# Performance work log

Measured on AMD Instinct MI355X. Metric: run time of the kernel, lower is better.

## Reference

```python
import jax, jax.numpy as jnp
import numpy as np

N, K, D = 65536, 4096, 64


def setup_inputs() -> dict:
    key = jax.random.key(0)
    kx, ke = jax.random.split(key)
    x = jax.random.normal(kx, (N, D), dtype=jnp.float32)
    embed = jax.random.normal(ke, (1, K, D), dtype=jnp.float32)
    return {"x": x, "embed": embed}


def reference(x, embed):
    # Faithful to EuclideanCodebook.forward quantization path:
    #   dist = cdist(flatten, embed, p=2)**2 ; argmin ; one_hot @ embed
    xf = x.astype(jnp.float32)            # [N, D]
    e = embed[0]                          # [K, D]
    # squared euclidean distance via expansion (== cdist(...).pow(2))
    x_sq = jnp.sum(xf * xf, axis=-1, keepdims=True)        # [N, 1]
    e_sq = jnp.sum(e * e, axis=-1)                          # [K]
    dist = jnp.maximum(x_sq + e_sq[None, :] - 2.0 * (xf @ e.T), 0.0)  # [N, K]
    embed_ind = jnp.argmin(dist, axis=-1)                   # [N]
    # one_hot @ embed is exactly a row gather of the codebook
    quantize = e[embed_ind]                                 # [N, D]
    return quantize, embed_ind[None, :]                     # embed_ind kept as [1, N] like torch
```

## Files before the change

### kernel.cpp

```cpp
#include <hip/hip_runtime.h>
#include <math.h>

#define N_ROWS 65536
#define K_CODES 4096
#define NTILES_TOTAL (K_CODES / 32)
#define K_CHUNKS 2
#define NTILES (NTILES_TOTAL / K_CHUNKS)
#define DIM 64
#define NBUF 4
#define ACC_MARGIN 0.005f

typedef __attribute__((ext_vector_type(8))) short bf16x8;
typedef __attribute__((ext_vector_type(16))) float f32x16;

__device__ inline unsigned short f2bf_rne(float f) {
    unsigned u = __float_as_uint(f);
    return (unsigned short)((u + 0x7FFFu + ((u >> 16) & 1u)) >> 16);
}
__device__ inline float bf2f(unsigned short s) {
    return __uint_as_float(((unsigned)s) << 16);
}

__global__ __launch_bounds__(256) void pack_e(const float* __restrict__ embed,
                                              short* __restrict__ e_pk,
                                              float* __restrict__ esq,
                                              float* __restrict__ esqn,
                                              int* __restrict__ count) {
    __shared__ float lds_f[2048];
    const int tile = blockIdx.x;
    const int t = threadIdx.x;
    if (tile == 0 && t == 0) *count = 0;
    const float4* src = (const float4*)(embed + (size_t)tile * 2048);
    ((float4*)lds_f)[t] = src[t];
    ((float4*)lds_f)[t + 256] = src[t + 256];
    __syncthreads();
    const int l = t & 63, ks = t >> 6;
    const int base = (l & 31) * 64 + ks * 16 + (l >> 5) * 8;
    bf16x8 vh, vl;
#pragma unroll
    for (int j = 0; j < 8; ++j) {
        float v = lds_f[base + j];
        unsigned short h = f2bf_rne(v);
        vh[j] = (short)h;
        vl[j] = (short)f2bf_rne(v - bf2f(h));
    }
    *(bf16x8*)(e_pk + (size_t)tile * 4096 + t * 8) = vh;
    *(bf16x8*)(e_pk + (size_t)tile * 4096 + 2048 + t * 8) = vl;
    if (t < 32) {
        float s = 0.f;
#pragma unroll
        for (int d = 0; d < 64; ++d) { float v = lds_f[t * 64 + d]; s = fmaf(v, v, s); }
        esq[tile * 32 + t] = s;
        esqn[tile * 32 + t] = -0.5f * s;
    }
}

__global__ __launch_bounds__(256, 4) void vq_main(const float* __restrict__ x,
                                                  const short* __restrict__ e_pk,
                                                  const float* __restrict__ esqn,
                                                  float* __restrict__ b1s,
                                                  float* __restrict__ b2s,
                                                  int* __restrict__ i1s) {
    __shared__ __align__(16) char lds[NBUF][8192];
    __shared__ __align__(16) float lds_q[NBUF][64];
    const int tid = threadIdx.x;
    const int wid = tid >> 6;
    const int l = tid & 63;
    const int col = l & 31;
    const int g = l >> 5;
    const int kc = blockIdx.x & (K_CHUNKS - 1);
    const int rg = blockIdx.x >> 1;
    const int rowbase = rg * 128 + wid * 32;
    const int tile0 = kc * NTILES;

    const float* xrow = x + (size_t)(rowbase + col) * DIM;
    bf16x8 ah[4], al[4];
#pragma unroll
    for (int ks = 0; ks < 4; ++ks) {
        const float* p = xrow + ks * 16 + g * 8;
#pragma unroll
        for (int j = 0; j < 8; ++j) {
            float v = p[j];
            unsigned short h = f2bf_rne(v);
            ah[ks][j] = (short)h;
            al[ks][j] = (short)f2bf_rne(v - bf2f(h));
        }
    }

    float b1[16], b2[16];
    int i1[16];
#pragma unroll
    for (int i = 0; i < 16; ++i) { b1[i] = -3.0e38f; b2[i] = -3.0e38f; i1[i] = 0; }

    auto stage = [&](int t, int b) {
        const char* gsrc = (const char*)e_pk + (size_t)(tile0 + t) * 8192 + tid * 16;
        __builtin_amdgcn_global_load_lds(
            (const __attribute__((address_space(1))) void*)gsrc,
            (__attribute__((address_space(3))) void*)(&lds[b][wid * 1024]), 16, 0, 0);
        __builtin_amdgcn_global_load_lds(
            (const __attribute__((address_space(1))) void*)(gsrc + 4096),
            (__attribute__((address_space(3))) void*)(&lds[b][4096 + wid * 1024]), 16, 0, 0);
        const float* qsrc = esqn + (size_t)(tile0 + t) * 32 + l;
        __builtin_amdgcn_global_load_lds(
            (const __attribute__((address_space(1))) void*)qsrc,
            (__attribute__((address_space(3))) void*)(&lds_q[b][0]), 4, 0, 0);
    };

    stage(0, 0);
    stage(1, 1);

    for (int t = 0; t < NTILES; ++t) {
        const int cur = t & (NBUF - 1);
        if (t + 2 < NTILES) stage(t + 2, (t + 2) & (NBUF - 1));
        asm volatile("s_waitcnt vmcnt(6)" ::: "memory");
        __builtin_amdgcn_sched_barrier(0);
        __builtin_amdgcn_s_barrier();
        __builtin_amdgcn_sched_barrier(0);

        const float esqn_v = lds_q[cur][col];
        const int cidx = (tile0 + t) * 32 + col;

        f32x16 acc;
#pragma unroll
        for (int i = 0; i < 16; ++i) acc[i] = esqn_v;

        __builtin_amdgcn_s_setprio(1);
#pragma unroll
        for (int ks = 0; ks < 4; ++ks) {
            const bf16x8 bh = *(const bf16x8*)(&lds[cur][(ks * 64 + l) * 16]);
            const bf16x8 bl = *(const bf16x8*)(&lds[cur][4096 + (ks * 64 + l) * 16]);
            acc = __builtin_amdgcn_mfma_f32_32x32x16_bf16(ah[ks], bh, acc, 0, 0, 0);
            acc = __builtin_amdgcn_mfma_f32_32x32x16_bf16(ah[ks], bl, acc, 0, 0, 0);
            acc = __builtin_amdgcn_mfma_f32_32x32x16_bf16(al[ks], bh, acc, 0, 0, 0);
        }
        __builtin_amdgcn_s_setprio(0);

#pragma unroll
        for (int i = 0; i < 16; ++i) {
            float val = acc[i];
            bool gt = val > b1[i];
            b2[i] = __builtin_amdgcn_fmed3f(val, b1[i], b2[i]);
            b1[i] = fmaxf(val, b1[i]);
            i1[i] = gt ? cidx : i1[i];
        }
    }

#pragma unroll
    for (int i = 0; i < 16; ++i) {
#pragma unroll
        for (int m = 1; m <= 16; m <<= 1) {
            float ob1 = __shfl_xor(b1[i], m);
            float ob2 = __shfl_xor(b2[i], m);
            int oi = __shfl_xor(i1[i], m);
            float nb2 = fmaxf(fminf(b1[i], ob1), fmaxf(b2[i], ob2));
            bool take = ob1 > b1[i];
            b1[i] = take ? ob1 : b1[i];
            i1[i] = take ? oi : i1[i];
            b2[i] = nb2;
        }
        if (col == 0) {
            int row = rowbase + (i & 3) + 8 * (i >> 2) + 4 * g;
            b1s[(size_t)kc * N_ROWS + row] = b1[i];
            b2s[(size_t)kc * N_ROWS + row] = b2[i];
            i1s[(size_t)kc * N_ROWS + row] = i1[i];
        }
    }
}

__global__ __launch_bounds__(256) void vq_merge_gather(const float* __restrict__ embed,
                                                       const float* __restrict__ b1s,
                                                       const float* __restrict__ b2s,
                                                       const int* __restrict__ i1s,
                                                       float* __restrict__ out_q,
                                                       float* __restrict__ out_ind,
                                                       int* __restrict__ list,
                                                       int* __restrict__ count) {
    int t = blockIdx.x * 256 + threadIdx.x;
    int r = t >> 3, q = t & 7;
    float ab1 = b1s[r], bb1 = b1s[N_ROWS + r];
    float ab2 = b2s[r], bb2 = b2s[N_ROWS + r];
    int ai = i1s[r], bi = i1s[N_ROWS + r];
    bool take = bb1 > ab1;
    int idx = take ? bi : ai;
    float m1 = fmaxf(ab1, bb1);
    float m2 = fmaxf(fminf(ab1, bb1), fmaxf(ab2, bb2));
    const float4* src = (const float4*)(embed + (size_t)idx * DIM + q * 8);
    float4* dst = (float4*)(out_q + (size_t)r * DIM + q * 8);
    dst[0] = src[0];
    dst[1] = src[1];
    if (q == 0) {
        out_ind[r] = (float)idx;
        if (m1 - m2 < ACC_MARGIN) {
            int p = atomicAdd(count, 1);
            list[p] = r;
        }
    }
}

__global__ __launch_bounds__(256) void vq_rescore(const float* __restrict__ x,
                                                  const float* __restrict__ embed,
                                                  const float* __restrict__ esq,
                                                  const int* __restrict__ list,
                                                  const int* __restrict__ count,
                                                  float* __restrict__ out_q,
                                                  float* __restrict__ out_ind) {
    __shared__ float xs[64];
    __shared__ float sk[256];
    __shared__ int si[256];
    const int tid = threadIdx.x;
    const int n = *count;
    for (int f = blockIdx.x; f < n; f += gridDim.x) {
        const int row = list[f];
        if (tid < 16) ((float4*)xs)[tid] = ((const float4*)(x + (size_t)row * DIM))[tid];
        __syncthreads();
        float best = 3.0e38f;
        int bi = 0;
        for (int i = 0; i < 16; ++i) {
            int c = tid + (i << 8);
            const float* e = embed + (size_t)c * DIM;
            float d0 = 0, d1 = 0, d2 = 0, d3 = 0;
#pragma unroll
            for (int d = 0; d < 64; d += 4) {
                d0 = fmaf(xs[d + 0], e[d + 0], d0);
                d1 = fmaf(xs[d + 1], e[d + 1], d1);
                d2 = fmaf(xs[d + 2], e[d + 2], d2);
                d3 = fmaf(xs[d + 3], e[d + 3], d3);
            }
            float key = fmaf(-2.f, (d0 + d1) + (d2 + d3), esq[c]);
            if (key < best) { best = key; bi = c; }
        }
        sk[tid] = best; si[tid] = bi;
        __syncthreads();
        for (int s = 128; s > 0; s >>= 1) {
            if (tid < s) {
                float ok = sk[tid + s]; int oi = si[tid + s];
                if (ok < sk[tid] || (ok == sk[tid] && oi < si[tid])) { sk[tid] = ok; si[tid] = oi; }
            }
            __syncthreads();
        }
        if (tid == 0) out_ind[row] = (float)si[0];
        if (tid < 16) {
            const float4* src = (const float4*)(embed + (size_t)si[0] * DIM);
            ((float4*)(out_q + (size_t)row * DIM))[tid] = src[tid];
        }
        __syncthreads();
    }
}

extern "C" void kernel_launch(void* const* d_in, const int* in_sizes, int n_in,
                              void* d_out, int out_size, void* d_ws, size_t ws_size,
                              hipStream_t stream) {
    const float* x = (const float*)d_in[0];
    const float* embed = (const float*)d_in[1];
    float* out = (float*)d_out;
    float* out_ind = out + (size_t)N_ROWS * DIM;

    char* ws = (char*)d_ws;
    short* e_pk = (short*)ws;
    size_t off = 1 << 20;
    float* esq = (float*)(ws + off);  off += 17 << 10;
    float* esqn = (float*)(ws + off); off += 17 << 10;
    float* b1s = (float*)(ws + off);  off += (size_t)K_CHUNKS * N_ROWS * 4;
    float* b2s = (float*)(ws + off);  off += (size_t)K_CHUNKS * N_ROWS * 4;
    int* i1s = (int*)(ws + off);      off += (size_t)K_CHUNKS * N_ROWS * 4;
    int* list = (int*)(ws + off);     off += (size_t)N_ROWS * 4;
    int* count = (int*)(ws + off);

    pack_e<<<NTILES_TOTAL, 256, 0, stream>>>(embed, e_pk, esq, esqn, count);
    vq_main<<<(N_ROWS / 128) * K_CHUNKS, 256, 0, stream>>>(x, e_pk, esqn, b1s, b2s, i1s);
    vq_merge_gather<<<N_ROWS * 8 / 256, 256, 0, stream>>>(embed, b1s, b2s, i1s,
                                                          out, out_ind, list, count);
    vq_rescore<<<512, 256, 0, stream>>>(x, embed, esq, list, count, out, out_ind);
}
```

Baseline: 163.3 us.

## Switch distance MFMA from 32x32x16 to 16x16x32 tiles with repacked codebook layout

Replaces the 32x32x16 bf16 MFMA with four 16x16x32 MFMAs per tile, each covering a 16x16 row-code block. The codebook packing and x fragment loading are changed to match the new operand layout. The running top-2 tracking and cross-lane reduction are adapted, adding a final merge of the two column halves per row. The aim is to use an instruction shape with different latency and throughput characteristics and to shorten the shuffle reduction, at the cost of more instructions and more LDS fragment reads per tile.

```diff
diff --git a/kernel.cpp b/kernel.cpp
--- a/kernel.cpp
+++ b/kernel.cpp
@@ -11,7 +11,7 @@
 #define ACC_MARGIN 0.005f
 
 typedef __attribute__((ext_vector_type(8))) short bf16x8;
-typedef __attribute__((ext_vector_type(16))) float f32x16;
+typedef __attribute__((ext_vector_type(4))) float f32x4;
 
 __device__ inline unsigned short f2bf_rne(float f) {
     unsigned u = __float_as_uint(f);
@@ -34,8 +34,10 @@
     ((float4*)lds_f)[t] = src[t];
     ((float4*)lds_f)[t + 256] = src[t + 256];
     __syncthreads();
-    const int l = t & 63, ks = t >> 6;
-    const int base = (l & 31) * 64 + ks * 16 + (l >> 5) * 8;
+    const int l = t & 63;
+    const int kh = (t >> 6) & 1;
+    const int ch = (t >> 7) & 1;
+    const int base = (ch * 16 + (l & 15)) * 64 + kh * 32 + ((l >> 4) & 3) * 8;
     bf16x8 vh, vl;
 #pragma unroll
     for (int j = 0; j < 8; ++j) {
@@ -66,24 +68,27 @@
     const int tid = threadIdx.x;
     const int wid = tid >> 6;
     const int l = tid & 63;
-    const int col = l & 31;
-    const int g = l >> 5;
+    const int c16 = l & 15;
+    const int rgrp = (l >> 4) & 3;
     const int kc = blockIdx.x & (K_CHUNKS - 1);
     const int rg = blockIdx.x >> 1;
     const int rowbase = rg * 128 + wid * 32;
     const int tile0 = kc * NTILES;
 
-    const float* xrow = x + (size_t)(rowbase + col) * DIM;
-    bf16x8 ah[4], al[4];
-#pragma unroll
-    for (int ks = 0; ks < 4; ++ks) {
-        const float* p = xrow + ks * 16 + g * 8;
-#pragma unroll
-        for (int j = 0; j < 8; ++j) {
-            float v = p[j];
-            unsigned short h = f2bf_rne(v);
-            ah[ks][j] = (short)h;
-            al[ks][j] = (short)f2bf_rne(v - bf2f(h));
+    bf16x8 ah[2][2], al[2][2];
+#pragma unroll
+    for (int rh = 0; rh < 2; ++rh) {
+        const float* xr = x + (size_t)(rowbase + rh * 16 + c16) * DIM;
+#pragma unroll
+        for (int kh = 0; kh < 2; ++kh) {
+            const float* p = xr + kh * 32 + rgrp * 8;
+#pragma unroll
+            for (int j = 0; j < 8; ++j) {
+                float v = p[j];
+                unsigned short h = f2bf_rne(v);
+                ah[rh][kh][j] = (short)h;
+                al[rh][kh][j] = (short)f2bf_rne(v - bf2f(h));
+            }
         }
     }
 
@@ -117,53 +122,92 @@
         __builtin_amdgcn_s_barrier();
         __builtin_amdgcn_sched_barrier(0);
 
-        const float esqn_v = lds_q[cur][col];
-        const int cidx = (tile0 + t) * 32 + col;
-
-        f32x16 acc;
-#pragma unroll
-        for (int i = 0; i < 16; ++i) acc[i] = esqn_v;
+        const float eq0 = lds_q[cur][c16];
+        const float eq1 = lds_q[cur][16 + c16];
+        const int ci0 = (tile0 + t) * 32 + c16;
+        const int ci1 = ci0 + 16;
+
+        bf16x8 bh[2][2], bl[2][2];
+#pragma unroll
+        for (int ch = 0; ch < 2; ++ch)
+#pragma unroll
+            for (int kh = 0; kh < 2; ++kh) {
+                const int fo = ((ch * 2 + kh) * 64 + l) * 16;
+                bh[ch][kh] = *(const bf16x8*)(&lds[cur][fo]);
+                bl[ch][kh] = *(const bf16x8*)(&lds[cur][4096 + fo]);
+            }
+
+        f32x4 a00 = {eq0, eq0, eq0, eq0};
+        f32x4 a01 = {eq1, eq1, eq1, eq1};
+        f32x4 a10 = {eq0, eq0, eq0, eq0};
+        f32x4 a11 = {eq1, eq1, eq1, eq1};
 
         __builtin_amdgcn_s_setprio(1);
 #pragma unroll
-        for (int ks = 0; ks < 4; ++ks) {
-            const bf16x8 bh = *(const bf16x8*)(&lds[cur][(ks * 64 + l) * 16]);
-            const bf16x8 bl = *(const bf16x8*)(&lds[cur][4096 + (ks * 64 + l) * 16]);
-            acc = __builtin_amdgcn_mfma_f32_32x32x16_bf16(ah[ks], bh, acc, 0, 0, 0);
-            acc = __builtin_amdgcn_mfma_f32_32x32x16_bf16(ah[ks], bl, acc, 0, 0, 0);
-            acc = __builtin_amdgcn_mfma_f32_32x32x16_bf16(al[ks], bh, acc, 0, 0, 0);
+        for (int kh = 0; kh < 2; ++kh) {
+            a00 = __builtin_amdgcn_mfma_f32_16x16x32_bf16(ah[0][kh], bh[0][kh], a00, 0, 0, 0);
+            a01 = __builtin_amdgcn_mfma_f32_16x16x32_bf16(ah[0][kh], bh[1][kh], a01, 0, 0, 0);
+            a10 = __builtin_amdgcn_mfma_f32_16x16x32_bf16(ah[1][kh], bh[0][kh], a10, 0, 0, 0);
+            a11 = __builtin_amdgcn_mfma_f32_16x16x32_bf16(ah[1][kh], bh[1][kh], a11, 0, 0, 0);
+            a00 = __builtin_amdgcn_mfma_f32_16x16x32_bf16(ah[0][kh], bl[0][kh], a00, 0, 0, 0);
+            a01 = __builtin_amdgcn_mfma_f32_16x16x32_bf16(ah[0][kh], bl[1][kh], a01, 0, 0, 0);
+            a10 = __builtin_amdgcn_mfma_f32_16x16x32_bf16(ah[1][kh], bl[0][kh], a10, 0, 0, 0);
+            a11 = __builtin_amdgcn_mfma_f32_16x16x32_bf16(ah[1][kh], bl[1][kh], a11, 0, 0, 0);
+            a00 = __builtin_amdgcn_mfma_f32_16x16x32_bf16(al[0][kh], bh[0][kh], a00, 0, 0, 0);
+            a01 = __builtin_amdgcn_mfma_f32_16x16x32_bf16(al[0][kh], bh[1][kh], a01, 0, 0, 0);
+            a10 = __builtin_amdgcn_mfma_f32_16x16x32_bf16(al[1][kh], bh[0][kh], a10, 0, 0, 0);
+            a11 = __builtin_amdgcn_mfma_f32_16x16x32_bf16(al[1][kh], bh[1][kh], a11, 0, 0, 0);
         }
         __builtin_amdgcn_s_setprio(0);
 
-#pragma unroll
-        for (int i = 0; i < 16; ++i) {
-            float val = acc[i];
-            bool gt = val > b1[i];
-            b2[i] = __builtin_amdgcn_fmed3f(val, b1[i], b2[i]);
-            b1[i] = fmaxf(val, b1[i]);
-            i1[i] = gt ? cidx : i1[i];
-        }
-    }
-
-#pragma unroll
-    for (int i = 0; i < 16; ++i) {
-#pragma unroll
-        for (int m = 1; m <= 16; m <<= 1) {
-            float ob1 = __shfl_xor(b1[i], m);
-            float ob2 = __shfl_xor(b2[i], m);
-            int oi = __shfl_xor(i1[i], m);
-            float nb2 = fmaxf(fminf(b1[i], ob1), fmaxf(b2[i], ob2));
-            bool take = ob1 > b1[i];
-            b1[i] = take ? ob1 : b1[i];
-            i1[i] = take ? oi : i1[i];
-            b2[i] = nb2;
-        }
-        if (col == 0) {
-            int row = rowbase + (i & 3) + 8 * (i >> 2) + 4 * g;
-            b1s[(size_t)kc * N_ROWS + row] = b1[i];
-            b2s[(size_t)kc * N_ROWS + row] = b2[i];
-            i1s[(size_t)kc * N_ROWS + row] = i1[i];
-        }
+#define TRACK(ACC, Q, CIDX)                                         \
+        _Pragma("unroll")                                           \
+        for (int j = 0; j < 4; ++j) {                               \
+            float val = (ACC)[j];                                   \
+            int e = (Q) * 4 + j;                                    \
+            bool gt = val > b1[e];                                  \
+            b2[e] = __builtin_amdgcn_fmed3f(val, b1[e], b2[e]);     \
+            b1[e] = fmaxf(val, b1[e]);                              \
+            i1[e] = gt ? (CIDX) : i1[e];                            \
+        }
+        TRACK(a00, 0, ci0)
+        TRACK(a01, 1, ci1)
+        TRACK(a10, 2, ci0)
+        TRACK(a11, 3, ci1)
+#undef TRACK
+    }
+
+#pragma unroll
+    for (int e = 0; e < 16; ++e) {
+#pragma unroll
+        for (int m = 1; m <= 8; m <<= 1) {
+            float ob1 = __shfl_xor(b1[e], m);
+            float ob2 = __shfl_xor(b2[e], m);
+            int oi = __shfl_xor(i1[e], m);
+            float nb2 = fmaxf(fminf(b1[e], ob1), fmaxf(b2[e], ob2));
+            bool take = ob1 > b1[e];
+            b1[e] = take ? ob1 : b1[e];
+            i1[e] = take ? oi : i1[e];
+            b2[e] = nb2;
+        }
+    }
+
+    if (c16 == 0) {
+#pragma unroll
+        for (int rh = 0; rh < 2; ++rh)
+#pragma unroll
+            for (int j = 0; j < 4; ++j) {
+                int ea = (rh * 2 + 0) * 4 + j;
+                int eb = (rh * 2 + 1) * 4 + j;
+                bool take = b1[eb] > b1[ea];
+                float m1 = fmaxf(b1[ea], b1[eb]);
+                float m2 = fmaxf(fminf(b1[ea], b1[eb]), fmaxf(b2[ea], b2[eb]));
+                int idx = take ? i1[eb] : i1[ea];
+                int row = rowbase + rh * 16 + rgrp * 4 + j;
+                b1s[(size_t)kc * N_ROWS + row] = m1;
+                b2s[(size_t)kc * N_ROWS + row] = m2;
+                i1s[(size_t)kc * N_ROWS + row] = idx;
+            }
     }
 }
 
```

New measurement: 238.2 us. +45.8%, slower.
